# Performance work log

Measured on AMD Instinct MI355X. Metric: run time of the kernel, lower is better.

Reference implementation:

```python
import jax, jax.numpy as jnp
import numpy as np

B, L, E, H, T = 8, 4096, 512, 8, 2
D = E // H


def setup_inputs() -> dict:
    key = jax.random.key(0)
    ks = jax.random.split(key, 11)
    s = 0.02
    return {
        "query": jax.random.normal(ks[0], (B, L, E), jnp.float32),
        "key": jax.random.normal(ks[1], (B, L, E), jnp.float32),
        "value": jax.random.normal(ks[2], (B, L, E), jnp.float32),
        "Wq": jax.random.normal(ks[3], (T, E, E), jnp.float32) * s,
        "bq": jax.random.normal(ks[4], (T, E), jnp.float32) * s,
        "Wk": jax.random.normal(ks[5], (T, E, E), jnp.float32) * s,
        "bk": jax.random.normal(ks[6], (T, E), jnp.float32) * s,
        "Wv": jax.random.normal(ks[7], (E, E), jnp.float32) * s,
        "bv": jax.random.normal(ks[8], (E,), jnp.float32) * s,
        "Wout": jax.random.normal(ks[9], (E, E), jnp.float32) * s,
        "bout": jax.random.normal(ks[10], (E,), jnp.float32) * s,
    }


def reference(query, key, value, Wq, bq, Wk, bk, Wv, bv, Wout, bout):
    bsz, tgt_len, embed_dim = query.shape
    src_len = key.shape[1]
    n_head = H
    head_dim = embed_dim // n_head

    # value projection: (B,S,H,D)
    v = (value @ Wv.T + bv).reshape(bsz, src_len, n_head, head_dim)
    # faithful to torch: value.view(-1, bsz*n_head, head_dim).transpose(0,1)
    # WITHOUT permuting to (S,B,H,D) first -> pure memory reinterpretation
    v = jnp.swapaxes(v.reshape(src_len, bsz * n_head, head_dim), 0, 1)  # (BH,S,D)

    # per-term q/k projections -> (T,L,B,H,D) / (T,S,B,H,D)
    q = jnp.einsum('ble,tfe->tblf', query, Wq) + bq[:, None, None, :]
    k = jnp.einsum('bse,tfe->tbsf', key, Wk) + bk[:, None, None, :]
    q = q.reshape(T, bsz, tgt_len, n_head, head_dim).transpose(0, 2, 1, 3, 4)
    k = k.reshape(T, bsz, src_len, n_head, head_dim).transpose(0, 2, 1, 3, 4)

    # act_fun == softmax: q softmax over feature dim, k softmax over sequence dim (dim 0)
    q = jax.nn.softmax(q, axis=-1)
    k = jax.nn.softmax(k, axis=1)

    # flatten: (T, L, B*H, D) -> (T, B*H, L, D)
    q = jnp.swapaxes(q.reshape(T, tgt_len, bsz * n_head, head_dim), 1, 2)
    k = jnp.swapaxes(k.reshape(T, src_len, bsz * n_head, head_dim), 1, 2)

    # cosine positional reweighting (cosFormer): doubles feature dim
    m = max(src_len, tgt_len)
    idx = (np.pi / 2) * jnp.arange(1, m + 1, dtype=q.dtype) / m  # (m,)
    sin_q = jnp.sin(idx[:tgt_len])[None, None, :, None]
    cos_q = jnp.cos(idx[:tgt_len])[None, None, :, None]
    sin_k = jnp.sin(idx[:src_len])[None, None, :, None]
    cos_k = jnp.cos(idx[:src_len])[None, None, :, None]
    q = jnp.concatenate([q * sin_q, q * cos_q], axis=-1)  # (T,BH,L,2D)
    k = jnp.concatenate([k * sin_k, k * cos_k], axis=-1)  # (T,BH,S,2D)

    # linear attention: kv state then output, summed over terms
    kv = jnp.einsum('tnsd,nsm->tndm', k, v)          # (T,BH,2D,D)
    out = jnp.einsum('tnld,tndm->nlm', q, kv)        # (BH,L,D) summed over T

    # back to (B,L,E)
    out = jnp.swapaxes(out, 0, 1).reshape(tgt_len, bsz, embed_dim)
    out = jnp.swapaxes(out, 0, 1)
    return out @ Wout.T + bout
```

## Files before the change

### kernel.cpp

```cpp
#include <hip/hip_runtime.h>
#include <cstdio>

#define E_DIM 512
#define L_DIM 4096
#define B_DIM 8
#define H_DIM 8
#define T_DIM 2
#define M_ROWS 32768

typedef __attribute__((ext_vector_type(8))) __bf16 bf16x8;
typedef __attribute__((ext_vector_type(4))) float f32x4;

static __device__ __forceinline__ unsigned short f2bf(float f) {
  unsigned int u = __float_as_uint(f);
  return (unsigned short)((u + 0x7FFFu + ((u >> 16) & 1u)) >> 16);
}
static __device__ __forceinline__ unsigned int pkbf(float lo, float hi) {
  return (unsigned int)f2bf(lo) | ((unsigned int)f2bf(hi) << 16);
}
static __device__ __forceinline__ float bf2f(unsigned short u) {
  return __uint_as_float((unsigned int)u << 16);
}
static __device__ __forceinline__ void unpk8(uint4 u, float* f) {
  f[0] = bf2f((unsigned short)u.x); f[1] = bf2f((unsigned short)(u.x >> 16));
  f[2] = bf2f((unsigned short)u.y); f[3] = bf2f((unsigned short)(u.y >> 16));
  f[4] = bf2f((unsigned short)u.z); f[5] = bf2f((unsigned short)(u.z >> 16));
  f[6] = bf2f((unsigned short)u.w); f[7] = bf2f((unsigned short)(u.w >> 16));
}
static __device__ __forceinline__ int swz64(int row, int e) {
  return row * 64 + ((((e >> 3) ^ row) & 7) << 3) + (e & 7);
}
static __device__ __forceinline__ int swz128(int row, int e) {
  return row * 128 + ((((e >> 3) ^ row) & 7) << 3) + ((e >> 3) & 8) * 8 + (e & 7);
}
static __device__ __forceinline__ void gl_lds16(const unsigned short* g,
                                                unsigned short* l) {
  __builtin_amdgcn_global_load_lds(
      (const __attribute__((address_space(1))) unsigned int*)g,
      (__attribute__((address_space(3))) unsigned int*)l, 16, 0, 0);
}

__global__ void sincos_kernel(float* __restrict__ sintab, float* __restrict__ costab) {
  int i = blockIdx.x * blockDim.x + threadIdx.x;
  if (i < L_DIM) {
    float idx = 1.57079632679489662f * (float)(i + 1) / (float)L_DIM;
    sintab[i] = sinf(idx);
    costab[i] = cosf(idx);
  }
}

__global__ void convf2b(const float* __restrict__ src, unsigned short* __restrict__ dst,
                        int n8) {
  for (int i = blockIdx.x * blockDim.x + threadIdx.x; i < n8; i += gridDim.x * blockDim.x) {
    float4 a = *(const float4*)(src + (size_t)i * 8);
    float4 b = *(const float4*)(src + (size_t)i * 8 + 4);
    uint4 o;
    o.x = pkbf(a.x, a.y); o.y = pkbf(a.z, a.w);
    o.z = pkbf(b.x, b.y); o.w = pkbf(b.z, b.w);
    *(uint4*)(dst + (size_t)i * 8) = o;
  }
}

#define YHALF 16777216
template <bool OUTF32, int NBL2>
__global__ __launch_bounds__(256) void gemm_xwt(
    const unsigned short* __restrict__ X, const unsigned short* __restrict__ W,
    const float* __restrict__ bias, void* __restrict__ Yv) {
  __shared__ __align__(16) unsigned short smem[17408];
  unsigned short* As = smem;
  unsigned short* Bs = smem + 8192;
  const int tid = threadIdx.x;
  const int id = blockIdx.x;
  const int j = id >> 3;
  const int mb = (id & 7) * 32 + (j >> NBL2);
  const int nb = j & ((1 << NBL2) - 1);
  const int m0 = mb * 128, n0 = nb * 128;
  const int lane = tid & 63;
  const int w = tid >> 6;
  const int wr = w >> 1, wc = w & 1;
  const int lr = lane & 15;
  const int lk = (lane >> 4) * 8;
  const int srow_off = lane >> 3;
  const int sp = lane & 7;
  f32x4 acc[4][4];
#pragma unroll
  for (int i = 0; i < 4; ++i)
#pragma unroll
    for (int jj = 0; jj < 4; ++jj) acc[i][jj] = (f32x4){0.f, 0.f, 0.f, 0.f};

  for (int k0 = 0; k0 < 512; k0 += 64) {
    __syncthreads();
#pragma unroll
    for (int i = 0; i < 4; ++i) {
      int rb = w * 32 + i * 8;
      int row = rb + srow_off;
      int gsrc = sp ^ (row & 7);
      gl_lds16(X + (size_t)(m0 + row) * 512 + k0 + gsrc * 8, &As[rb * 64]);
      gl_lds16(W + (size_t)(n0 + row) * 512 + k0 + gsrc * 8, &Bs[rb * 64]);
    }
    __syncthreads();
#pragma unroll
    for (int kk = 0; kk < 2; ++kk) {
      bf16x8 av[4], bv[4];
      int ke = kk * 32 + lk;
#pragma unroll
      for (int fm = 0; fm < 4; ++fm)
        av[fm] = *(const bf16x8*)&As[swz64(wr * 64 + fm * 16 + lr, ke)];
#pragma unroll
      for (int fn = 0; fn < 4; ++fn)
        bv[fn] = *(const bf16x8*)&Bs[swz64(wc * 64 + fn * 16 + lr, ke)];
#pragma unroll
      for (int fm = 0; fm < 4; ++fm)
#pragma unroll
        for (int fn = 0; fn < 4; ++fn)
          acc[fm][fn] = __builtin_amdgcn_mfma_f32_16x16x32_bf16(av[fm], bv[fn],
                                                                acc[fm][fn], 0, 0, 0);
    }
  }
  __syncthreads();
  const int rq = lane >> 4;
  if (!OUTF32) {
    unsigned short* Cs = smem;
#pragma unroll
    for (int fn = 0; fn < 4; ++fn) {
      int col = wc * 64 + fn * 16 + lr;
      float bb = bias[n0 + col];
#pragma unroll
      for (int fm = 0; fm < 4; ++fm) {
        int row = wr * 64 + fm * 16 + rq * 4;
#pragma unroll
        for (int jj = 0; jj < 4; ++jj)
          Cs[(row + jj) * 136 + col] = f2bf(acc[fm][fn][jj] + bb);
      }
    }
    __syncthreads();
    unsigned short* Yb = (unsigned short*)Yv + (size_t)(n0 >> 9) * YHALF;
    const int nc = n0 & 511;
#pragma unroll
    for (int i = 0; i < 8; ++i) {
      int idx = tid + i * 256;
      int row = idx >> 4, g = idx & 15;
      *(uint4*)(Yb + (size_t)(m0 + row) * 512 + nc + g * 8) =
          *(const uint4*)&Cs[row * 136 + g * 8];
    }
  } else {
    float* Cf = (float*)smem;
    float* Yf = (float*)Yv;
#pragma unroll
    for (int p = 0; p < 2; ++p) {
      if (p) __syncthreads();
      if (wr == p) {
#pragma unroll
        for (int fn = 0; fn < 4; ++fn) {
          int col = wc * 64 + fn * 16 + lr;
          float bb = bias[n0 + col];
#pragma unroll
          for (int fm = 0; fm < 4; ++fm) {
            int lrow = fm * 16 + rq * 4;
#pragma unroll
            for (int jj = 0; jj < 4; ++jj)
              Cf[(lrow + jj) * 132 + col] = acc[fm][fn][jj] + bb;
          }
        }
      }
      __syncthreads();
#pragma unroll
      for (int i = 0; i < 8; ++i) {
        int idx = tid + i * 256;
        int row = idx >> 5, g = idx & 31;
        *(float4*)(Yf + (size_t)(m0 + p * 64 + row) * 512 + n0 + g * 4) =
            *(const float4*)&Cf[row * 132 + g * 4];
      }
    }
  }
}

__global__ __launch_bounds__(256) void kcolstats_part(
    const unsigned short* __restrict__ Kp, float* __restrict__ pmax,
    float* __restrict__ psum) {
  int b = blockIdx.x;
  int chunk = blockIdx.y;
  int gx = threadIdx.x;
  int sy = threadIdx.y;
  const unsigned short* base = Kp + ((size_t)b * L_DIM + chunk * 128) * 512 + gx * 8;
  __shared__ float red[4][512];
  float m[8];
#pragma unroll
  for (int k = 0; k < 8; ++k) m[k] = -3.0e38f;
  for (int s = sy; s < 128; s += 4) {
    uint4 q = *(const uint4*)(base + (size_t)s * 512);
    float v[8];
    unpk8(q, v);
#pragma unroll
    for (int k = 0; k < 8; ++k) m[k] = fmaxf(m[k], v[k]);
  }
  *(float4*)&red[sy][gx * 8] = make_float4(m[0], m[1], m[2], m[3]);
  *(float4*)&red[sy][gx * 8 + 4] = make_float4(m[4], m[5], m[6], m[7]);
  __syncthreads();
#pragma unroll
  for (int k = 0; k < 8; ++k) {
    int f = gx * 8 + k;
    m[k] = fmaxf(fmaxf(red[0][f], red[1][f]), fmaxf(red[2][f], red[3][f]));
  }
  __syncthreads();
  float sum[8];
#pragma unroll
  for (int k = 0; k < 8; ++k) sum[k] = 0.f;
  for (int s = sy; s < 128; s += 4) {
    uint4 q = *(const uint4*)(base + (size_t)s * 512);
    float v[8];
    unpk8(q, v);
#pragma unroll
    for (int k = 0; k < 8; ++k) sum[k] += __expf(v[k] - m[k]);
  }
  *(float4*)&red[sy][gx * 8] = make_float4(sum[0], sum[1], sum[2], sum[3]);
  *(float4*)&red[sy][gx * 8 + 4] = make_float4(sum[4], sum[5], sum[6], sum[7]);
  __syncthreads();
  if (sy == 0) {
#pragma unroll
    for (int k = 0; k < 8; ++k) {
      int f = gx * 8 + k;
      float s = (red[0][f] + red[1][f]) + (red[2][f] + red[3][f]);
      pmax[(size_t)chunk * 4096 + b * E_DIM + f] = m[k];
      psum[(size_t)chunk * 4096 + b * E_DIM + f] = s;
    }
  }
}

__global__ void kcolstats_reduce(const float* __restrict__ pmax,
                                 const float* __restrict__ psum,
                                 float* __restrict__ colmax,
                                 float* __restrict__ colinv) {
  int i = blockIdx.x * 256 + threadIdx.x;
  float M = -3.0e38f, S = 0.f;
#pragma unroll
  for (int c = 0; c < 32; ++c) {
    float m = pmax[(size_t)c * 4096 + i];
    float s = psum[(size_t)c * 4096 + i];
    float nm = fmaxf(M, m);
    S = S * __expf(M - nm) + s * __expf(m - nm);
    M = nm;
  }
  colmax[i] = M;
  colinv[i] = 1.f / S;
}

__global__ __launch_bounds__(256) void kv_mfma(
    const unsigned short* __restrict__ Kp, const unsigned short* __restrict__ Vpb,
    const float* __restrict__ colmax, const float* __restrict__ colinv,
    const float* __restrict__ sintab, const float* __restrict__ costab,
    float* __restrict__ kvpart) {
  __shared__ __align__(16) unsigned short kT[64 * 64];
  __shared__ __align__(16) unsigned short vT[128 * 64];
  __shared__ float cmaxs[64], cinvs[64];
  const int tid = threadIdx.x;
  const int chunk = blockIdx.x;
  const int n = blockIdx.y;
  const int b = n >> 3, h = n & 7;
  if (tid < 64) {
    cmaxs[tid] = colmax[b * E_DIM + h * 64 + tid];
    cinvs[tid] = colinv[b * E_DIM + h * 64 + tid];
  }
  const int lane = tid & 63;
  const int w = tid >> 6;
  const int lr = lane & 15;
  const int lk = (lane >> 4) * 8;
  const int sp = tid & 31;
  const int g = tid >> 5;
  f32x4 acc[4][2];
#pragma unroll
  for (int i = 0; i < 4; ++i) {
    acc[i][0] = (f32x4){0.f, 0.f, 0.f, 0.f};
    acc[i][1] = (f32x4){0.f, 0.f, 0.f, 0.f};
  }
  __syncthreads();

  for (int st = 0; st < 8; ++st) {
    int sA = chunk * 512 + st * 64 + 2 * sp;
    const unsigned short* kp = Kp + ((size_t)b * L_DIM + sA) * 512 + h * 64 + g * 8;
    uint4 ka = *(const uint4*)kp;
    uint4 kb = *(const uint4*)(kp + 512);
    int vr = ((sA >> 9) << 12) + ((sA & 511) << 3) + b;
    const unsigned short* vp = Vpb + (size_t)vr * 512 + h * 64 + g * 8;
    uint4 v0 = *(const uint4*)vp;
    uint4 v1 = *(const uint4*)(vp + 8 * 512);
    float kfa[8], kfb[8], vA[8], vB[8];
    unpk8(ka, kfa);
    unpk8(kb, kfb);
    unpk8(v0, vA);
    unpk8(v1, vB);
    float sS = sintab[sA], sC = costab[sA];
    float tS = sintab[sA + 1], tC = costab[sA + 1];
    __syncthreads();
#pragma unroll
    for (int i = 0; i < 8; ++i) {
      int d = g * 8 + i;
      float e0 = __expf(kfa[i] - cmaxs[d]) * cinvs[d];
      float e1 = __expf(kfb[i] - cmaxs[d]) * cinvs[d];
      *(unsigned int*)&kT[swz64(d, 2 * sp)] = pkbf(e0, e1);
    }
#pragma unroll
    for (int i = 0; i < 8; ++i) {
      int m = g * 8 + i;
      *(unsigned int*)&vT[swz64(m, 2 * sp)] = pkbf(vA[i] * sS, vB[i] * tS);
      *(unsigned int*)&vT[swz64(64 + m, 2 * sp)] = pkbf(vA[i] * sC, vB[i] * tC);
    }
    __syncthreads();
#pragma unroll
    for (int kk = 0; kk < 2; ++kk) {
      int ke = kk * 32 + lk;
      bf16x8 av[4], bv[2];
#pragma unroll
      for (int fm = 0; fm < 4; ++fm)
        av[fm] = *(const bf16x8*)&kT[swz64(fm * 16 + lr, ke)];
#pragma unroll
      for (int fn = 0; fn < 2; ++fn)
        bv[fn] = *(const bf16x8*)&vT[swz64(w * 32 + fn * 16 + lr, ke)];
#pragma unroll
      for (int fm = 0; fm < 4; ++fm)
#pragma unroll
        for (int fn = 0; fn < 2; ++fn)
          acc[fm][fn] = __builtin_amdgcn_mfma_f32_16x16x32_bf16(av[fm], bv[fn],
                                                                acc[fm][fn], 0, 0, 0);
    }
  }
  const int rq = lane >> 4;
#pragma unroll
  for (int fn = 0; fn < 2; ++fn) {
    int ncol = w * 32 + fn * 16 + lr;
    int m = ncol & 63;
    int ddbase = (ncol >> 6) * 64;
#pragma unroll
    for (int fm = 0; fm < 4; ++fm) {
#pragma unroll
      for (int jj = 0; jj < 4; ++jj) {
        int dd = ddbase + fm * 16 + rq * 4 + jj;
        kvpart[(((size_t)chunk * 64 + n) * 64 + m) * 128 + dd] = acc[fm][fn][jj];
      }
    }
  }
}

__global__ void kv_reduce_swz(const float* __restrict__ part,
                              unsigned short* __restrict__ kvT) {
  int i = blockIdx.x * 256 + threadIdx.x;
  float s = 0.f;
#pragma unroll
  for (int c = 0; c < 8; ++c) s += part[(size_t)c * 524288 + i];
  int dd = i & 127;
  int m = (i >> 7) & 63;
  int nm = i >> 7;
  int gg = dd >> 3;
  int e = ((gg & 8) | ((gg ^ m) & 7)) * 8 + (dd & 7);
  kvT[(size_t)nm * 128 + e] = f2bf(s);
}

__global__ __launch_bounds__(256) void out_fused(
    const unsigned short* __restrict__ Qp0, const unsigned short* __restrict__ Qp1,
    const unsigned short* __restrict__ kvT,
    const float* __restrict__ sintab, const float* __restrict__ costab,
    unsigned short* __restrict__ Yb) {
  __shared__ __align__(16) unsigned short q2s[64 * 128];
  __shared__ __align__(16) unsigned short kvs[2][64 * 128];
  const int tid = threadIdx.x;
  const int lc = blockIdx.x;
  const int n = blockIdx.y;
  const int b = n >> 3, h = n & 7;
  const int lane = tid & 63;
  const int w = tid >> 6;
  {
    const uint4* s0 = (const uint4*)(kvT + (size_t)n * 8192);
    const uint4* s1 = (const uint4*)(kvT + 524288 + (size_t)n * 8192);
    uint4* d0 = (uint4*)kvs[0];
    uint4* d1 = (uint4*)kvs[1];
#pragma unroll
    for (int i = 0; i < 4; ++i) {
      d0[tid + i * 256] = s0[tid + i * 256];
      d1[tid + i * 256] = s1[tid + i * 256];
    }
  }
  const int l0 = lc * 64;
  const int wr = w >> 1, wc = w & 1;
  const int lr = lane & 15;
  const int lk = (lane >> 4) * 8;
  const int rq = lane >> 4;
  f32x4 acc[2][2];
  acc[0][0] = acc[0][1] = acc[1][0] = acc[1][1] = (f32x4){0.f, 0.f, 0.f, 0.f};
#pragma unroll
  for (int t = 0; t < 2; ++t) {
    const unsigned short* Qp = t ? Qp1 : Qp0;
    if (t) __syncthreads();
#pragma unroll
    for (int i = 0; i < 2; ++i) {
      int idx = tid + i * 256;
      int row = idx >> 3;
      int g = idx & 7;
      uint4 q = *(const uint4*)(Qp + ((size_t)b * L_DIM + l0 + row) * 512 +
                                h * 64 + g * 8);
      float v[8];
      unpk8(q, v);
      float m8 = fmaxf(fmaxf(fmaxf(v[0], v[1]), fmaxf(v[2], v[3])),
                       fmaxf(fmaxf(v[4], v[5]), fmaxf(v[6], v[7])));
      m8 = fmaxf(m8, __shfl_xor(m8, 1));
      m8 = fmaxf(m8, __shfl_xor(m8, 2));
      m8 = fmaxf(m8, __shfl_xor(m8, 4));
      float e[8], s8;
#pragma unroll
      for (int k = 0; k < 8; ++k) e[k] = __expf(v[k] - m8);
      s8 = ((e[0] + e[1]) + (e[2] + e[3])) + ((e[4] + e[5]) + (e[6] + e[7]));
      s8 += __shfl_xor(s8, 1);
      s8 += __shfl_xor(s8, 2);
      s8 += __shfl_xor(s8, 4);
      float inv = 1.f / s8;
      int gl = l0 + row;
      float sn = sintab[gl] * inv;
      float cs = costab[gl] * inv;
      uint4 os, oc;
      os.x = pkbf(e[0] * sn, e[1] * sn); os.y = pkbf(e[2] * sn, e[3] * sn);
      os.z = pkbf(e[4] * sn, e[5] * sn); os.w = pkbf(e[6] * sn, e[7] * sn);
      oc.x = pkbf(e[0] * cs, e[1] * cs); oc.y = pkbf(e[2] * cs, e[3] * cs);
      oc.z = pkbf(e[4] * cs, e[5] * cs); oc.w = pkbf(e[6] * cs, e[7] * cs);
      *(uint4*)&q2s[swz128(row, g * 8)] = os;
      *(uint4*)&q2s[swz128(row, 64 + g * 8)] = oc;
    }
    __syncthreads();
#pragma unroll
    for (int ks = 0; ks < 4; ++ks) {
      int ke = ks * 32 + lk;
      bf16x8 av[2], bv[2];
#pragma unroll
      for (int fm = 0; fm < 2; ++fm)
        av[fm] = *(const bf16x8*)&q2s[swz128(wr * 32 + fm * 16 + lr, ke)];
#pragma unroll
      for (int fn = 0; fn < 2; ++fn)
        bv[fn] = *(const bf16x8*)&kvs[t][swz128(wc * 32 + fn * 16 + lr, ke)];
#pragma unroll
      for (int fm = 0; fm < 2; ++fm)
#pragma unroll
        for (int fn = 0; fn < 2; ++fn)
          acc[fm][fn] = __builtin_amdgcn_mfma_f32_16x16x32_bf16(av[fm], bv[fn],
                                                                acc[fm][fn], 0, 0, 0);
    }
  }
  __syncthreads();
  unsigned short* Os = q2s;
#pragma unroll
  for (int fn = 0; fn < 2; ++fn) {
    int col = wc * 32 + fn * 16 + lr;
#pragma unroll
    for (int fm = 0; fm < 2; ++fm) {
      int lrow = wr * 32 + fm * 16 + rq * 4;
#pragma unroll
      for (int jj = 0; jj < 4; ++jj)
        Os[(lrow + jj) * 72 + col] = f2bf(acc[fm][fn][jj]);
    }
  }
  __syncthreads();
#pragma unroll
  for (int i = 0; i < 2; ++i) {
    int idx = tid + i * 256;
    int row = idx >> 3, g = idx & 7;
    *(uint4*)(Yb + ((size_t)b * L_DIM + l0 + row) * 512 + h * 64 + g * 8) =
        *(const uint4*)&Os[row * 72 + g * 8];
  }
}

extern "C" void kernel_launch(void* const* d_in, const int* in_sizes, int n_in,
                              void* d_out, int out_size, void* d_ws, size_t ws_size,
                              hipStream_t stream) {
  const float* query = (const float*)d_in[0];
  const float* key   = (const float*)d_in[1];
  const float* value = (const float*)d_in[2];
  const float* Wq    = (const float*)d_in[3];
  const float* bq    = (const float*)d_in[4];
  const float* Wk    = (const float*)d_in[5];
  const float* bk    = (const float*)d_in[6];
  const float* Wv    = (const float*)d_in[7];
  const float* bv    = (const float*)d_in[8];
  const float* Wout  = (const float*)d_in[9];
  const float* bout  = (const float*)d_in[10];
  float* out = (float*)d_out;
  float* ws = (float*)d_ws;

  const size_t F_PROJ0 = 0;
  const size_t F_PROJ1 = F_PROJ0 + 8388608;
  const size_t F_VPB   = F_PROJ1 + 8388608;
  const size_t F_KVP   = F_VPB + 8388608;
  const size_t F_KVT   = F_KVP + 4194304;
  const size_t F_XBUF  = F_KVT + 524288;
  const size_t F_WBF   = F_XBUF + 8388608;
  const size_t F_CMAX  = F_WBF + 786432;
  const size_t F_CINV  = F_CMAX + 4096;
  const size_t F_SIN   = F_CINV + 4096;
  const size_t F_COS   = F_SIN + 4096;
  const size_t TOTALF  = F_COS + 4096;
  if (ws_size < TOTALF * sizeof(float)) {
    fprintf(stderr, "kernel_launch: ws too small (%zu < %zu)\n", ws_size, TOTALF * 4);
    return;
  }
  unsigned short* proj0 = (unsigned short*)(ws + F_PROJ0);
  unsigned short* vpb   = (unsigned short*)(ws + F_VPB);
  float* kvpart = ws + F_KVP;
  unsigned short* kvT  = (unsigned short*)(ws + F_KVT);
  unsigned short* xbuf = (unsigned short*)(ws + F_XBUF);
  unsigned short* wbf  = (unsigned short*)(ws + F_WBF);
  float* cmax = ws + F_CMAX;
  float* cinv = ws + F_CINV;
  float* sintab = ws + F_SIN;
  float* costab = ws + F_COS;
  float* pmax = kvpart;
  float* psum = kvpart + 131072;
  const size_t WQ_O = 0, WK_O = 524288, WV_O = 1048576, WOUT_O = 1310720;

  sincos_kernel<<<16, 256, 0, stream>>>(sintab, costab);
  convf2b<<<256, 256, 0, stream>>>(Wq, wbf + WQ_O, 65536);
  convf2b<<<256, 256, 0, stream>>>(Wk, wbf + WK_O, 65536);
  convf2b<<<128, 256, 0, stream>>>(Wv, wbf + WV_O, 32768);
  convf2b<<<128, 256, 0, stream>>>(Wout, wbf + WOUT_O, 32768);

  convf2b<<<2048, 256, 0, stream>>>(value, xbuf, 2097152);
  gemm_xwt<false, 2><<<1024, 256, 0, stream>>>(xbuf, wbf + WV_O, bv, vpb);

  convf2b<<<2048, 256, 0, stream>>>(key, xbuf, 2097152);
  gemm_xwt<false, 3><<<2048, 256, 0, stream>>>(xbuf, wbf + WK_O, bk, proj0);
  for (int t = 0; t < T_DIM; ++t) {
    unsigned short* projt = proj0 + (size_t)t * YHALF;
    kcolstats_part<<<dim3(8, 32), dim3(64, 4), 0, stream>>>(projt, pmax, psum);
    kcolstats_reduce<<<16, 256, 0, stream>>>(pmax, psum, cmax, cinv);
    kv_mfma<<<dim3(8, 64), 256, 0, stream>>>(projt, vpb, cmax, cinv,
                                             sintab, costab, kvpart);
    kv_reduce_swz<<<2048, 256, 0, stream>>>(kvpart, kvT + (size_t)t * 524288);
  }

  convf2b<<<2048, 256, 0, stream>>>(query, xbuf, 2097152);
  gemm_xwt<false, 3><<<2048, 256, 0, stream>>>(xbuf, wbf + WQ_O, bq, proj0);
  out_fused<<<dim3(64, 64), 256, 0, stream>>>(proj0, proj0 + YHALF, kvT,
                                              sintab, costab, xbuf);
  gemm_xwt<true, 2><<<1024, 256, 0, stream>>>(xbuf, wbf + WOUT_O, bout, out);
}
```

Measured before the change: 364.6 us.

## Fuse key softmax column stats into K-projection GEMM and double-buffer LDS

The K-projection GEMM epilogue now computes per-tile column max and sum-of-exp from fp32 accumulators, so the separate column-stats passes that reread the projected keys are gone. A single reduce per term combines the partials. The GEMM main loop also gains double-buffered LDS with prefetch of the next k-slice, overlapping global loads with MFMA work. LDS use doubles, which may reduce occupancy, and the stats now come from pre-rounding values.

```diff
diff --git a/kernel.cpp b/kernel.cpp
--- a/kernel.cpp
+++ b/kernel.cpp
@@ -62,13 +62,12 @@
 }
 
 #define YHALF 16777216
-template <bool OUTF32, int NBL2>
+template <bool OUTF32, bool STATS, int NBL2>
 __global__ __launch_bounds__(256) void gemm_xwt(
     const unsigned short* __restrict__ X, const unsigned short* __restrict__ W,
-    const float* __restrict__ bias, void* __restrict__ Yv) {
-  __shared__ __align__(16) unsigned short smem[17408];
-  unsigned short* As = smem;
-  unsigned short* Bs = smem + 8192;
+    const float* __restrict__ bias, void* __restrict__ Yv,
+    float* __restrict__ pmax, float* __restrict__ psum) {
+  __shared__ __align__(16) unsigned short smem[32768];
   const int tid = threadIdx.x;
   const int id = blockIdx.x;
   const int j = id >> 3;
@@ -80,25 +79,39 @@
   const int wr = w >> 1, wc = w & 1;
   const int lr = lane & 15;
   const int lk = (lane >> 4) * 8;
-  const int srow_off = lane >> 3;
-  const int sp = lane & 7;
+  const int rq = lane >> 4;
+  const int srow = lane >> 3;
+  const int gsrc8 = ((lane & 7) ^ srow) * 8;
   f32x4 acc[4][4];
 #pragma unroll
   for (int i = 0; i < 4; ++i)
 #pragma unroll
     for (int jj = 0; jj < 4; ++jj) acc[i][jj] = (f32x4){0.f, 0.f, 0.f, 0.f};
 
-  for (int k0 = 0; k0 < 512; k0 += 64) {
-    __syncthreads();
-#pragma unroll
-    for (int i = 0; i < 4; ++i) {
-      int rb = w * 32 + i * 8;
-      int row = rb + srow_off;
-      int gsrc = sp ^ (row & 7);
-      gl_lds16(X + (size_t)(m0 + row) * 512 + k0 + gsrc * 8, &As[rb * 64]);
-      gl_lds16(W + (size_t)(n0 + row) * 512 + k0 + gsrc * 8, &Bs[rb * 64]);
-    }
-    __syncthreads();
+#pragma unroll
+  for (int i = 0; i < 4; ++i) {
+    int rb = w * 32 + i * 8;
+    gl_lds16(X + (size_t)(m0 + rb + srow) * 512 + gsrc8, &smem[rb * 64]);
+    gl_lds16(W + (size_t)(n0 + rb + srow) * 512 + gsrc8, &smem[8192 + rb * 64]);
+  }
+  __syncthreads();
+
+#pragma unroll
+  for (int step = 0; step < 8; ++step) {
+    const int cur = step & 1;
+    if (step < 7) {
+      unsigned short* Ab = smem + (cur ^ 1) * 16384;
+      const int kn = (step + 1) * 64;
+#pragma unroll
+      for (int i = 0; i < 4; ++i) {
+        int rb = w * 32 + i * 8;
+        gl_lds16(X + (size_t)(m0 + rb + srow) * 512 + kn + gsrc8, &Ab[rb * 64]);
+        gl_lds16(W + (size_t)(n0 + rb + srow) * 512 + kn + gsrc8,
+                 &Ab[8192 + rb * 64]);
+      }
+    }
+    const unsigned short* As = smem + cur * 16384;
+    const unsigned short* Bs = As + 8192;
 #pragma unroll
     for (int kk = 0; kk < 2; ++kk) {
       bf16x8 av[4], bv[4];
@@ -116,9 +129,47 @@
           acc[fm][fn] = __builtin_amdgcn_mfma_f32_16x16x32_bf16(av[fm], bv[fn],
                                                                 acc[fm][fn], 0, 0, 0);
     }
-  }
-  __syncthreads();
-  const int rq = lane >> 4;
+    __syncthreads();
+  }
+
+  if (STATS) {
+    float* sf = (float*)smem;
+#pragma unroll
+    for (int fn = 0; fn < 4; ++fn) {
+      float M = -3.0e38f;
+#pragma unroll
+      for (int fm = 0; fm < 4; ++fm)
+#pragma unroll
+        for (int jj = 0; jj < 4; ++jj) M = fmaxf(M, acc[fm][fn][jj]);
+      M = fmaxf(M, __shfl_xor(M, 16));
+      M = fmaxf(M, __shfl_xor(M, 32));
+      float S = 0.f;
+#pragma unroll
+      for (int fm = 0; fm < 4; ++fm)
+#pragma unroll
+        for (int jj = 0; jj < 4; ++jj) S += __expf(acc[fm][fn][jj] - M);
+      S += __shfl_xor(S, 16);
+      S += __shfl_xor(S, 32);
+      if (rq == 0) {
+        int col = wc * 64 + fn * 16 + lr;
+        sf[wr * 128 + col] = M;
+        sf[256 + wr * 128 + col] = S;
+      }
+    }
+    __syncthreads();
+    if (tid < 128) {
+      float M0 = sf[tid], M1 = sf[128 + tid];
+      float S0 = sf[256 + tid], S1 = sf[384 + tid];
+      float nm = fmaxf(M0, M1);
+      float S = S0 * __expf(M0 - nm) + S1 * __expf(M1 - nm);
+      int gc = n0 + tid;
+      size_t mtile = (size_t)(m0 >> 7);
+      pmax[mtile * (128 << NBL2) + gc] = nm + bias[gc];
+      psum[mtile * (128 << NBL2) + gc] = S;
+    }
+    __syncthreads();
+  }
+
   if (!OUTF32) {
     unsigned short* Cs = smem;
 #pragma unroll
@@ -175,68 +226,18 @@
   }
 }
 
-__global__ __launch_bounds__(256) void kcolstats_part(
-    const unsigned short* __restrict__ Kp, float* __restrict__ pmax,
-    float* __restrict__ psum) {
-  int b = blockIdx.x;
-  int chunk = blockIdx.y;
-  int gx = threadIdx.x;
-  int sy = threadIdx.y;
-  const unsigned short* base = Kp + ((size_t)b * L_DIM + chunk * 128) * 512 + gx * 8;
-  __shared__ float red[4][512];
-  float m[8];
-#pragma unroll
-  for (int k = 0; k < 8; ++k) m[k] = -3.0e38f;
-  for (int s = sy; s < 128; s += 4) {
-    uint4 q = *(const uint4*)(base + (size_t)s * 512);
-    float v[8];
-    unpk8(q, v);
-#pragma unroll
-    for (int k = 0; k < 8; ++k) m[k] = fmaxf(m[k], v[k]);
-  }
-  *(float4*)&red[sy][gx * 8] = make_float4(m[0], m[1], m[2], m[3]);
-  *(float4*)&red[sy][gx * 8 + 4] = make_float4(m[4], m[5], m[6], m[7]);
-  __syncthreads();
-#pragma unroll
-  for (int k = 0; k < 8; ++k) {
-    int f = gx * 8 + k;
-    m[k] = fmaxf(fmaxf(red[0][f], red[1][f]), fmaxf(red[2][f], red[3][f]));
-  }
-  __syncthreads();
-  float sum[8];
-#pragma unroll
-  for (int k = 0; k < 8; ++k) sum[k] = 0.f;
-  for (int s = sy; s < 128; s += 4) {
-    uint4 q = *(const uint4*)(base + (size_t)s * 512);
-    float v[8];
-    unpk8(q, v);
-#pragma unroll
-    for (int k = 0; k < 8; ++k) sum[k] += __expf(v[k] - m[k]);
-  }
-  *(float4*)&red[sy][gx * 8] = make_float4(sum[0], sum[1], sum[2], sum[3]);
-  *(float4*)&red[sy][gx * 8 + 4] = make_float4(sum[4], sum[5], sum[6], sum[7]);
-  __syncthreads();
-  if (sy == 0) {
-#pragma unroll
-    for (int k = 0; k < 8; ++k) {
-      int f = gx * 8 + k;
-      float s = (red[0][f] + red[1][f]) + (red[2][f] + red[3][f]);
-      pmax[(size_t)chunk * 4096 + b * E_DIM + f] = m[k];
-      psum[(size_t)chunk * 4096 + b * E_DIM + f] = s;
-    }
-  }
-}
-
 __global__ void kcolstats_reduce(const float* __restrict__ pmax,
                                  const float* __restrict__ psum,
                                  float* __restrict__ colmax,
-                                 float* __restrict__ colinv) {
+                                 float* __restrict__ colinv, int coloff) {
   int i = blockIdx.x * 256 + threadIdx.x;
+  int b = i >> 9, f = i & 511;
   float M = -3.0e38f, S = 0.f;
 #pragma unroll
   for (int c = 0; c < 32; ++c) {
-    float m = pmax[(size_t)c * 4096 + i];
-    float s = psum[(size_t)c * 4096 + i];
+    size_t mt = (size_t)(b * 32 + c);
+    float m = pmax[mt * 1024 + coloff + f];
+    float s = psum[mt * 1024 + coloff + f];
     float nm = fmaxf(M, m);
     S = S * __expf(M - nm) + s * __expf(m - nm);
     M = nm;
@@ -490,8 +491,8 @@
   const size_t F_XBUF  = F_KVT + 524288;
   const size_t F_WBF   = F_XBUF + 8388608;
   const size_t F_CMAX  = F_WBF + 786432;
-  const size_t F_CINV  = F_CMAX + 4096;
-  const size_t F_SIN   = F_CINV + 4096;
+  const size_t F_CINV  = F_CMAX + 8192;
+  const size_t F_SIN   = F_CINV + 8192;
   const size_t F_COS   = F_SIN + 4096;
   const size_t TOTALF  = F_COS + 4096;
   if (ws_size < TOTALF * sizeof(float)) {
@@ -509,7 +510,7 @@
   float* sintab = ws + F_SIN;
   float* costab = ws + F_COS;
   float* pmax = kvpart;
-  float* psum = kvpart + 131072;
+  float* psum = kvpart + 262144;
   const size_t WQ_O = 0, WK_O = 524288, WV_O = 1048576, WOUT_O = 1310720;
 
   sincos_kernel<<<16, 256, 0, stream>>>(sintab, costab);
@@ -519,22 +520,27 @@
   convf2b<<<128, 256, 0, stream>>>(Wout, wbf + WOUT_O, 32768);
 
   convf2b<<<2048, 256, 0, stream>>>(value, xbuf, 2097152);
-  gemm_xwt<false, 2><<<1024, 256, 0, stream>>>(xbuf, wbf + WV_O, bv, vpb);
+  gemm_xwt<false, false, 2><<<1024, 256, 0, stream>>>(xbuf, wbf + WV_O, bv, vpb,
+                                                      nullptr, nullptr);
 
   convf2b<<<2048, 256, 0, stream>>>(key, xbuf, 2097152);
-  gemm_xwt<false, 3><<<2048, 256, 0, stream>>>(xbuf, wbf + WK_O, bk, proj0);
+  gemm_xwt<false, true, 3><<<2048, 256, 0, stream>>>(xbuf, wbf + WK_O, bk, proj0,
+                                                     pmax, psum);
+  kcolstats_reduce<<<16, 256, 0, stream>>>(pmax, psum, cmax, cinv, 0);
+  kcolstats_reduce<<<16, 256, 0, stream>>>(pmax, psum, cmax + 4096, cinv + 4096, 512);
   for (int t = 0; t < T_DIM; ++t) {
     unsigned short* projt = proj0 + (size_t)t * YHALF;
-    kcolstats_part<<<dim3(8, 32), dim3(64, 4), 0, stream>>>(projt, pmax, psum);
-    kcolstats_reduce<<<16, 256, 0, stream>>>(pmax, psum, cmax, cinv);
-    kv_mfma<<<dim3(8, 64), 256, 0, stream>>>(projt, vpb, cmax, cinv,
-                                             sintab, costab, kvpart);
+    kv_mfma<<<dim3(8, 64), 256, 0, stream>>>(projt, vpb, cmax + t * 4096,
+                                             cinv + t * 4096, sintab, costab,
+                                             kvpart);
     kv_reduce_swz<<<2048, 256, 0, stream>>>(kvpart, kvT + (size_t)t * 524288);
   }
 
   convf2b<<<2048, 256, 0, stream>>>(query, xbuf, 2097152);
-  gemm_xwt<false, 3><<<2048, 256, 0, stream>>>(xbuf, wbf + WQ_O, bq, proj0);
+  gemm_xwt<false, false, 3><<<2048, 256, 0, stream>>>(xbuf, wbf + WQ_O, bq, proj0,
+                                                      nullptr, nullptr);
   out_fused<<<dim3(64, 64), 256, 0, stream>>>(proj0, proj0 + YHALF, kvT,
                                               sintab, costab, xbuf);
-  gemm_xwt<true, 2><<<1024, 256, 0, stream>>>(xbuf, wbf + WOUT_O, bout, out);
-}
+  gemm_xwt<true, false, 2><<<1024, 256, 0, stream>>>(xbuf, wbf + WOUT_O, bout, out,
+                                                     nullptr, nullptr);
+}
```

Measured after the change: 325.8 us. 10.6% less time.
